# Optimization experiments

Hardware: AMD Instinct MI355X
Metric: run time of the kernel (lower is better)

## Reference

```python
import jax, jax.numpy as jnp
import numpy as np

EPS = 1e-12  # matches torch F.normalize default eps

def l2norm(t):
    n = jnp.linalg.norm(t, axis=-1, keepdims=True)
    return t / jnp.maximum(n, EPS)

def rotate_half(x):
    # '... (j d) -> ... j d' with j=2: split into two halves, return cat(-x2, x1)
    x1, x2 = jnp.split(x, 2, axis=-1)
    return jnp.concatenate((-x2, x1), axis=-1)

def rotary_freqs(seq_len, dim):
    inv_freq = 1.0 / (10000.0 ** (jnp.arange(0, dim, 2, dtype=jnp.float32) / dim))
    seq = jnp.arange(seq_len, dtype=jnp.float32)
    freqs = seq[:, None] * inv_freq[None, :]          # [n, d/2]
    emb = jnp.concatenate((freqs, freqs), axis=-1)    # [n, d]
    return emb[None, None]                            # [1, 1, n, d]

def apply_rotary_pos_emb(t, freqs):
    # rot_dim == dim_head here, so the pass-through slice is empty
    return t * jnp.cos(freqs) + rotate_half(t) * jnp.sin(freqs)

def setup_inputs() -> dict:
    key = jax.random.key(0)
    kq, kk, kv = jax.random.split(key, 3)
    b, h, n, d = 2, 16, 2048, 64
    q = jax.random.normal(kq, (b, h, n, d), dtype=jnp.float32)
    k = jax.random.normal(kk, (b, h, n, d), dtype=jnp.float32)
    v = jax.random.normal(kv, (b, h, n, d), dtype=jnp.float32)
    q_scale = jnp.ones((d,), dtype=jnp.float32)
    k_scale = jnp.ones((d,), dtype=jnp.float32)
    return {"q": q, "k": k, "v": v, "q_scale": q_scale, "k_scale": k_scale}

def reference(q, k, v, q_scale, k_scale):
    b, h, n, d = q.shape
    # QK RMSNorm (l2 normalize + learned per-dim scale)
    q = l2norm(q) * q_scale
    k = l2norm(k) * k_scale
    # rotary position embedding (always applied in the source module)
    freqs = rotary_freqs(n, d)
    q = apply_rotary_pos_emb(q, freqs)
    k = apply_rotary_pos_emb(k, freqs)
    # attention: explicit scores -> softmax -> values
    scale = d ** -0.5
    sim = jnp.einsum('bhid,bhjd->bhij', q, k) * scale
    attn = jax.nn.softmax(sim, axis=-1)
    out = jnp.einsum('bhij,bhjd->bhid', attn, v)
    # 'b h n d -> b n (h d)'
    return out.transpose(0, 2, 1, 3).reshape(b, n, h * d)
```

## Files before the change

kernel.cpp:

```cpp
#include <hip/hip_runtime.h>
#include <math.h>

#define BH   32
#define NSEQ 2048
#define DH   64
#define NH   16
#define LOG2E 1.44269504088896f

typedef _Float16 f16x8 __attribute__((ext_vector_type(8)));
typedef __fp16   fp16x2 __attribute__((ext_vector_type(2)));
typedef float    f32x16v __attribute__((ext_vector_type(16)));
typedef unsigned uint2v __attribute__((ext_vector_type(2)));

#if __has_builtin(__builtin_amdgcn_exp2f)
#define EXP2F(x) __builtin_amdgcn_exp2f(x)
#else
#define EXP2F(x) exp2f(x)
#endif

static __device__ __forceinline__ unsigned pkrtz(float a, float b) {
    fp16x2 r = __builtin_amdgcn_cvt_pkrtz(a, b);
    return __builtin_bit_cast(unsigned, r);
}
static __device__ __forceinline__ unsigned packh_rne(float a, float b) {
    union { _Float16 h[2]; unsigned u; } x;
    x.h[0] = (_Float16)a; x.h[1] = (_Float16)b;
    return x.u;
}
#if __has_builtin(__builtin_amdgcn_perm)
#define PERM(a, b, s) __builtin_amdgcn_perm((a), (b), (s))
#else
static __device__ __forceinline__ unsigned PERM(unsigned a, unsigned b, unsigned s) {
    if (s == 0x05040100u) return (b & 0xffffu) | (a << 16);
    return (b >> 16) | (a & 0xffff0000u);
}
#endif

static __device__ __forceinline__ float2 rope_cs(int pos, int p) {
    float invf_rev = EXP2F(-(float)p * (13.287712379549449f / 32.0f)) * 0.15915494309189535f;
    float rev = (float)pos * invf_rev;
    float fr = rev - floorf(rev);
    float th = fr * 6.283185307179586f;
    return make_float2(__cosf(th), __sinf(th));
}

__global__ __launch_bounds__(256) void prep_all(
    const float* __restrict__ q, const float* __restrict__ k, const float* __restrict__ v,
    const float* __restrict__ qs, const float* __restrict__ ksc,
    unsigned* __restrict__ qh, unsigned* __restrict__ kh, unsigned* __restrict__ vt2) {
    const int bid = blockIdx.x;
    const int t = threadIdx.x;
    if (bid < 16384) {
        const bool isq = bid < 8192;
        const float* in = isq ? q : k;
        const float* sc = isq ? qs : ksc;
        unsigned* outp  = isq ? qh : kh;
        const float smul = isq ? 0.125f * LOG2E : 1.0f;
        const int sb = bid & 8191;
        const int w = t >> 6, lane = t & 63;
        const int c = lane & 31, hfr = lane >> 5;
        const int row = sb * 8 + w * 2 + hfr;
        float2 x2 = *(const float2*)(in + (size_t)row * DH + 2 * c);
        float ss = x2.x * x2.x + x2.y * x2.y;
        #pragma unroll
        for (int off = 16; off > 0; off >>= 1) ss += __shfl_xor(ss, off);
        float inv = 1.0f / fmaxf(sqrtf(ss), 1e-12f);
        float2 s2 = *(const float2*)(sc + 2 * c);
        float t0 = x2.x * inv * s2.x;
        float t1 = x2.y * inv * s2.y;
        float p0 = __shfl_xor(t0, 16);
        float p1 = __shfl_xor(t1, 16);
        float r0 = (c < 16) ? -p0 : p0;
        float r1 = (c < 16) ? -p1 : p1;
        int pos = row & (NSEQ - 1);
        int pp = (2 * c) & 31;
        float2 cs0 = rope_cs(pos, pp);
        float2 cs1 = rope_cs(pos, pp + 1);
        float o0 = (t0 * cs0.x + r0 * cs0.y) * smul;
        float o1 = (t1 * cs1.x + r1 * cs1.y) * smul;
        outp[row * 32 + c] = packh_rne(o0, o1);
    } else {
        const int sb = bid - 16384;
        const int kt = sb & 31, bh = sb >> 5;
        __shared__ float Lv[64 * 68];
        #pragma unroll
        for (int i = 0; i < 4; ++i) {
            int chunk = t + 256 * i;
            int r = chunk >> 4, fg = chunk & 15;
            *(float4*)&Lv[r * 68 + fg * 4] =
                *(const float4*)(v + ((size_t)bh * NSEQ + kt * 64 + r) * DH + fg * 4);
        }
        __syncthreads();
        const int dp = t >> 3, kg = t & 7;
        unsigned u[8];
        #pragma unroll
        for (int j = 0; j < 8; ++j) {
            int key = kg * 8 + j;
            float2 f2 = *(const float2*)&Lv[key * 68 + 2 * dp];
            u[j] = pkrtz(f2.x, f2.y);
        }
        unsigned* dst = vt2 + ((size_t)bh * 32 + dp) * NSEQ + kt * 64 + kg * 8;
        *(uint4*)(dst + 0) = make_uint4(u[0], u[1], u[2], u[3]);
        *(uint4*)(dst + 4) = make_uint4(u[4], u[5], u[6], u[7]);
    }
}

__global__ __launch_bounds__(256, 4) void attn_kernel(
    const unsigned* __restrict__ qh, const unsigned* __restrict__ khg,
    const unsigned* __restrict__ vt2, float* __restrict__ out) {

    __shared__ _Float16 Ks[2][64 * 72];
    __shared__ _Float16 Vs[2][64 * 72];

    const int bh = blockIdx.y, qb = blockIdx.x;
    const int tid = threadIdx.x;
    const int w = tid >> 6, lane = tid & 63;
    const int c = lane & 31, hf = lane >> 5;
    const int qhw = w & 1;
    const int khw = w >> 1;

    const _Float16* qbase = (const _Float16*)qh + ((size_t)bh * NSEQ + qb * 64) * DH;
    const _Float16* kbase = (const _Float16*)khg + (size_t)bh * NSEQ * DH;
    const unsigned* vbase = vt2 + (size_t)bh * 32 * NSEQ;

    #pragma unroll
    for (int i = 0; i < 2; ++i) {
        int chunk = tid + 256 * i;
        int r = chunk >> 3, sg = chunk & 7;
        *(uint4*)&Ks[0][r * 72 + sg * 8] = *(const uint4*)(kbase + r * DH + sg * 8);
    }
    #pragma unroll
    for (int i = 0; i < 2; ++i) {
        int chunk = tid + 256 * i;
        int dp = chunk >> 4, kq = (chunk & 15) * 4;
        uint4 vr = *(const uint4*)(vbase + (size_t)dp * NSEQ + kq);
        uint2 lo, hi;
        lo.x = PERM(vr.y, vr.x, 0x05040100u); hi.x = PERM(vr.y, vr.x, 0x07060302u);
        lo.y = PERM(vr.w, vr.z, 0x05040100u); hi.y = PERM(vr.w, vr.z, 0x07060302u);
        *(uint2*)&Vs[0][(2 * dp) * 72 + kq]     = lo;
        *(uint2*)&Vs[0][(2 * dp + 1) * 72 + kq] = hi;
    }

    f16x8 qf[4];
    #pragma unroll
    for (int ks = 0; ks < 4; ++ks)
        qf[ks] = *(const f16x8*)(qbase + (qhw * 32 + c) * DH + ks * 16 + hf * 8);

    f32x16v o[2];
    #pragma unroll
    for (int mt = 0; mt < 2; ++mt)
        #pragma unroll
        for (int r = 0; r < 16; ++r) o[mt][r] = 0.f;
    float lpart = 0.f;

    __syncthreads();

    for (int jt = 0; jt < 32; ++jt) {
        const int cur = jt & 1;
        uint4 kpre[2], vpre[2];
        if (jt + 1 < 32) {
            #pragma unroll
            for (int i = 0; i < 2; ++i) {
                int chunk = tid + 256 * i;
                int r = chunk >> 3, sg = chunk & 7;
                kpre[i] = *(const uint4*)(kbase + (size_t)(jt + 1) * 64 * DH + r * DH + sg * 8);
            }
            #pragma unroll
            for (int i = 0; i < 2; ++i) {
                int chunk = tid + 256 * i;
                int dp = chunk >> 4, kq = (chunk & 15) * 4;
                vpre[i] = *(const uint4*)(vbase + (size_t)dp * NSEQ + (jt + 1) * 64 + kq);
            }
        }

        f32x16v s;
        #pragma unroll
        for (int r = 0; r < 16; ++r) s[r] = 0.f;
        #pragma unroll
        for (int ks = 0; ks < 4; ++ks) {
            f16x8 ka = *(const f16x8*)&Ks[cur][(khw * 32 + c) * 72 + ks * 16 + hf * 8];
            s = __builtin_amdgcn_mfma_f32_32x32x16_f16(ka, qf[ks], s, 0, 0, 0);
        }

        #pragma unroll
        for (int r = 0; r < 16; ++r) {
            float pv = EXP2F(s[r]);
            s[r] = pv;
            lpart += pv;
        }

        #pragma unroll
        for (int kk = 0; kk < 2; ++kk) {
            unsigned P01 = pkrtz(s[kk * 8 + 0], s[kk * 8 + 1]);
            unsigned P23 = pkrtz(s[kk * 8 + 2], s[kk * 8 + 3]);
            unsigned P45 = pkrtz(s[kk * 8 + 4], s[kk * 8 + 5]);
            unsigned P67 = pkrtz(s[kk * 8 + 6], s[kk * 8 + 7]);
            union { unsigned u[4]; f16x8 v; } B;
#if __has_builtin(__builtin_amdgcn_permlane32_swap)
            uint2v r02 = __builtin_amdgcn_permlane32_swap(P01, P45, 0, 0);
            uint2v r13 = __builtin_amdgcn_permlane32_swap(P23, P67, 0, 0);
            B.u[0] = r02[0]; B.u[1] = r13[0]; B.u[2] = r02[1]; B.u[3] = r13[1];
#else
            unsigned x01 = (unsigned)__shfl_xor((int)P01, 32);
            unsigned x23 = (unsigned)__shfl_xor((int)P23, 32);
            unsigned x45 = (unsigned)__shfl_xor((int)P45, 32);
            unsigned x67 = (unsigned)__shfl_xor((int)P67, 32);
            B.u[0] = hf ? x45 : P01;
            B.u[1] = hf ? x67 : P23;
            B.u[2] = hf ? P45 : x01;
            B.u[3] = hf ? P67 : x23;
#endif
            const int kc = khw * 2 + kk;
            f16x8 va0 = *(const f16x8*)&Vs[cur][c * 72 + kc * 16 + hf * 8];
            f16x8 va1 = *(const f16x8*)&Vs[cur][(32 + c) * 72 + kc * 16 + hf * 8];
            o[0] = __builtin_amdgcn_mfma_f32_32x32x16_f16(va0, B.v, o[0], 0, 0, 0);
            o[1] = __builtin_amdgcn_mfma_f32_32x32x16_f16(va1, B.v, o[1], 0, 0, 0);
        }

        if (jt + 1 < 32) {
            #pragma unroll
            for (int i = 0; i < 2; ++i) {
                int chunk = tid + 256 * i;
                int r = chunk >> 3, sg = chunk & 7;
                *(uint4*)&Ks[1 - cur][r * 72 + sg * 8] = kpre[i];
            }
            #pragma unroll
            for (int i = 0; i < 2; ++i) {
                int chunk = tid + 256 * i;
                int dp = chunk >> 4, kq = (chunk & 15) * 4;
                uint2 lo, hi;
                lo.x = PERM(vpre[i].y, vpre[i].x, 0x05040100u); hi.x = PERM(vpre[i].y, vpre[i].x, 0x07060302u);
                lo.y = PERM(vpre[i].w, vpre[i].z, 0x05040100u); hi.y = PERM(vpre[i].w, vpre[i].z, 0x07060302u);
                *(uint2*)&Vs[1 - cur][(2 * dp) * 72 + kq]     = lo;
                *(uint2*)&Vs[1 - cur][(2 * dp + 1) * 72 + kq] = hi;
            }
        }
        __syncthreads();
    }

    float lw = lpart + __shfl_xor(lpart, 32);
    float* Lred = (float*)&Ks[0][0];
    if (w >= 2) {
        const int base = ((w - 2) * 64 + lane) * 33;
        #pragma unroll
        for (int mt = 0; mt < 2; ++mt)
            #pragma unroll
            for (int r = 0; r < 16; ++r) Lred[base + mt * 16 + r] = o[mt][r];
        Lred[base + 32] = lw;
    }
    __syncthreads();
    if (w < 2) {
        const int base = (w * 64 + lane) * 33;
        #pragma unroll
        for (int mt = 0; mt < 2; ++mt)
            #pragma unroll
            for (int r = 0; r < 16; ++r) o[mt][r] += Lred[base + mt * 16 + r];
        lw += Lred[base + 32];
        float invl = 1.0f / lw;
        const int b = bh >> 4, h = bh & 15;
        const int pos = qb * 64 + w * 32 + c;
        float* obase = out + ((size_t)b * NSEQ + pos) * (NH * DH) + h * DH;
        #pragma unroll
        for (int mt = 0; mt < 2; ++mt)
            #pragma unroll
            for (int g = 0; g < 4; ++g) {
                float4 r4 = make_float4(o[mt][g * 4 + 0] * invl, o[mt][g * 4 + 1] * invl,
                                        o[mt][g * 4 + 2] * invl, o[mt][g * 4 + 3] * invl);
                *(float4*)(obase + mt * 32 + g * 8 + hf * 4) = r4;
            }
    }
}

extern "C" void kernel_launch(void* const* d_in, const int* in_sizes, int n_in,
                              void* d_out, int out_size, void* d_ws, size_t ws_size,
                              hipStream_t stream) {
    const float* q  = (const float*)d_in[0];
    const float* k  = (const float*)d_in[1];
    const float* v  = (const float*)d_in[2];
    const float* qs = (const float*)d_in[3];
    const float* ks = (const float*)d_in[4];
    float* outp = (float*)d_out;

    unsigned* qh  = (unsigned*)d_ws;
    unsigned* kh  = qh + (size_t)BH * NSEQ * 32;
    unsigned* vt2 = kh + (size_t)BH * NSEQ * 32;

    prep_all<<<17408, 256, 0, stream>>>(q, k, v, qs, ks, qh, kh, vt2);
    attn_kernel<<<dim3(NSEQ / 64, BH), 256, 0, stream>>>(qh, kh, vt2, outp);
}
```

Measured before the change: 149.0 us.

## Pre-swizzle K and V into MFMA fragment order and load directly to registers

The prep kernel now writes K and transposed V in an MFMA-operand-ready layout, so each lane can load its fragments from global memory with contiguous 16-byte loads. That lets the attention kernel drop the LDS staging buffers, the PERM shuffles and the per-tile __syncthreads, and register double-buffering replaces the shared-memory double buffer. The grid is also flattened and remapped so that blocks sharing a head are spread across groups, and the occupancy hint drops from 4 to 3 to leave room for the extra registers. Each wave now fetches its K/V fragments separately and relies on L2/cache reuse instead of LDS sharing, which increases global load traffic.

Result: faster. 144.6 us (-3.0%).

```diff
diff --git a/kernel.cpp b/kernel.cpp
--- a/kernel.cpp
+++ b/kernel.cpp
@@ -27,14 +27,6 @@
     x.h[0] = (_Float16)a; x.h[1] = (_Float16)b;
     return x.u;
 }
-#if __has_builtin(__builtin_amdgcn_perm)
-#define PERM(a, b, s) __builtin_amdgcn_perm((a), (b), (s))
-#else
-static __device__ __forceinline__ unsigned PERM(unsigned a, unsigned b, unsigned s) {
-    if (s == 0x05040100u) return (b & 0xffffu) | (a << 16);
-    return (b >> 16) | (a & 0xffff0000u);
-}
-#endif
 
 static __device__ __forceinline__ float2 rope_cs(int pos, int p) {
     float invf_rev = EXP2F(-(float)p * (13.287712379549449f / 32.0f)) * 0.15915494309189535f;
@@ -54,7 +46,6 @@
         const bool isq = bid < 8192;
         const float* in = isq ? q : k;
         const float* sc = isq ? qs : ksc;
-        unsigned* outp  = isq ? qh : kh;
         const float smul = isq ? 0.125f * LOG2E : 1.0f;
         const int sb = bid & 8191;
         const int w = t >> 6, lane = t & 63;
@@ -78,7 +69,15 @@
         float2 cs1 = rope_cs(pos, pp + 1);
         float o0 = (t0 * cs0.x + r0 * cs0.y) * smul;
         float o1 = (t1 * cs1.x + r1 * cs1.y) * smul;
-        outp[row * 32 + c] = packh_rne(o0, o1);
+        unsigned val = packh_rne(o0, o1);
+        if (isq) {
+            qh[row * 32 + c] = val;
+        } else {
+            const int rloc = row & (NSEQ - 1);
+            const unsigned idx = (unsigned)((rloc >> 5) * 1024 + (c >> 3) * 256
+                               + ((c >> 2) & 1) * 128 + (rloc & 31) * 4 + (c & 3));
+            kh[(size_t)(row >> 11) * 65536 + idx] = val;
+        }
     } else {
         const int sb = bid - 16384;
         const int kt = sb & 31, bh = sb >> 5;
@@ -91,28 +90,87 @@
                 *(const float4*)(v + ((size_t)bh * NSEQ + kt * 64 + r) * DH + fg * 4);
         }
         __syncthreads();
-        const int dp = t >> 3, kg = t & 7;
+        const int d = t & 63, kg = t >> 6;
         unsigned u[8];
         #pragma unroll
         for (int j = 0; j < 8; ++j) {
-            int key = kg * 8 + j;
-            float2 f2 = *(const float2*)&Lv[key * 68 + 2 * dp];
-            u[j] = pkrtz(f2.x, f2.y);
+            int ky = kg * 16 + 2 * j;
+            u[j] = pkrtz(Lv[ky * 68 + d], Lv[(ky + 1) * 68 + d]);
         }
-        unsigned* dst = vt2 + ((size_t)bh * 32 + dp) * NSEQ + kt * 64 + kg * 8;
-        *(uint4*)(dst + 0) = make_uint4(u[0], u[1], u[2], u[3]);
-        *(uint4*)(dst + 4) = make_uint4(u[4], u[5], u[6], u[7]);
-    }
-}
-
-__global__ __launch_bounds__(256, 4) void attn_kernel(
-    const unsigned* __restrict__ qh, const unsigned* __restrict__ khg,
-    const unsigned* __restrict__ vt2, float* __restrict__ out) {
-
-    __shared__ _Float16 Ks[2][64 * 72];
-    __shared__ _Float16 Vs[2][64 * 72];
-
-    const int bh = blockIdx.y, qb = blockIdx.x;
+        const int rh = d >> 5, cc = d & 31;
+        unsigned* dst = vt2 + (size_t)bh * 65536
+                      + (size_t)((kt * 4 + kg) * 2 + rh) * 256 + cc * 4;
+        *(uint4*)(dst)       = make_uint4(u[0], u[1], u[2], u[3]);
+        *(uint4*)(dst + 128) = make_uint4(u[4], u[5], u[6], u[7]);
+    }
+}
+
+static __device__ __forceinline__ f16x8 ld8(const unsigned* p) {
+    return *(const f16x8*)p;
+}
+
+static __device__ __forceinline__ void attn_step(
+    const f16x8 (&kc)[4], const f16x8 (&vc)[4],
+    f16x8 (&kn)[4], f16x8 (&vn)[4],
+    const unsigned* kp, const unsigned* vp, bool pre,
+    const f16x8 (&qf)[4], f32x16v (&o)[2], float& lpart, int hf)
+{
+    if (pre) {
+        #pragma unroll
+        for (int ks = 0; ks < 4; ++ks) kn[ks] = ld8(kp + ks * 256);
+        #pragma unroll
+        for (int kk = 0; kk < 2; ++kk)
+            #pragma unroll
+            for (int rh = 0; rh < 2; ++rh)
+                vn[kk * 2 + rh] = ld8(vp + kk * 512 + rh * 256);
+    }
+    f32x16v s;
+    #pragma unroll
+    for (int r = 0; r < 16; ++r) s[r] = 0.f;
+    #pragma unroll
+    for (int ks = 0; ks < 4; ++ks)
+        s = __builtin_amdgcn_mfma_f32_32x32x16_f16(kc[ks], qf[ks], s, 0, 0, 0);
+    #pragma unroll
+    for (int r = 0; r < 16; ++r) {
+        float pv = EXP2F(s[r]);
+        s[r] = pv;
+        lpart += pv;
+    }
+    #pragma unroll
+    for (int kk = 0; kk < 2; ++kk) {
+        unsigned P01 = pkrtz(s[kk * 8 + 0], s[kk * 8 + 1]);
+        unsigned P23 = pkrtz(s[kk * 8 + 2], s[kk * 8 + 3]);
+        unsigned P45 = pkrtz(s[kk * 8 + 4], s[kk * 8 + 5]);
+        unsigned P67 = pkrtz(s[kk * 8 + 6], s[kk * 8 + 7]);
+        union { unsigned u[4]; f16x8 v; } B;
+#if __has_builtin(__builtin_amdgcn_permlane32_swap)
+        uint2v r02 = __builtin_amdgcn_permlane32_swap(P01, P45, 0, 0);
+        uint2v r13 = __builtin_amdgcn_permlane32_swap(P23, P67, 0, 0);
+        B.u[0] = r02[0]; B.u[1] = r13[0]; B.u[2] = r02[1]; B.u[3] = r13[1];
+#else
+        unsigned x01 = (unsigned)__shfl_xor((int)P01, 32);
+        unsigned x23 = (unsigned)__shfl_xor((int)P23, 32);
+        unsigned x45 = (unsigned)__shfl_xor((int)P45, 32);
+        unsigned x67 = (unsigned)__shfl_xor((int)P67, 32);
+        B.u[0] = hf ? x45 : P01;
+        B.u[1] = hf ? x67 : P23;
+        B.u[2] = hf ? P45 : x01;
+        B.u[3] = hf ? P67 : x23;
+#endif
+        o[0] = __builtin_amdgcn_mfma_f32_32x32x16_f16(vc[kk * 2 + 0], B.v, o[0], 0, 0, 0);
+        o[1] = __builtin_amdgcn_mfma_f32_32x32x16_f16(vc[kk * 2 + 1], B.v, o[1], 0, 0, 0);
+    }
+}
+
+__global__ __launch_bounds__(256, 3) void attn_kernel(
+    const unsigned* __restrict__ qh, const unsigned* __restrict__ kf,
+    const unsigned* __restrict__ vf, float* __restrict__ out) {
+
+    __shared__ float Lred[128 * 33];
+
+    const int flat = (blockIdx.x & 7) * 128 + (blockIdx.x >> 3);
+    const int bh = flat >> 5, qb = flat & 31;
+
     const int tid = threadIdx.x;
     const int w = tid >> 6, lane = tid & 63;
     const int c = lane & 31, hf = lane >> 5;
@@ -120,32 +178,23 @@
     const int khw = w >> 1;
 
     const _Float16* qbase = (const _Float16*)qh + ((size_t)bh * NSEQ + qb * 64) * DH;
-    const _Float16* kbase = (const _Float16*)khg + (size_t)bh * NSEQ * DH;
-    const unsigned* vbase = vt2 + (size_t)bh * 32 * NSEQ;
-
-    #pragma unroll
-    for (int i = 0; i < 2; ++i) {
-        int chunk = tid + 256 * i;
-        int r = chunk >> 3, sg = chunk & 7;
-        *(uint4*)&Ks[0][r * 72 + sg * 8] = *(const uint4*)(kbase + r * DH + sg * 8);
-    }
-    #pragma unroll
-    for (int i = 0; i < 2; ++i) {
-        int chunk = tid + 256 * i;
-        int dp = chunk >> 4, kq = (chunk & 15) * 4;
-        uint4 vr = *(const uint4*)(vbase + (size_t)dp * NSEQ + kq);
-        uint2 lo, hi;
-        lo.x = PERM(vr.y, vr.x, 0x05040100u); hi.x = PERM(vr.y, vr.x, 0x07060302u);
-        lo.y = PERM(vr.w, vr.z, 0x05040100u); hi.y = PERM(vr.w, vr.z, 0x07060302u);
-        *(uint2*)&Vs[0][(2 * dp) * 72 + kq]     = lo;
-        *(uint2*)&Vs[0][(2 * dp + 1) * 72 + kq] = hi;
-    }
-
     f16x8 qf[4];
     #pragma unroll
     for (int ks = 0; ks < 4; ++ks)
         qf[ks] = *(const f16x8*)(qbase + (qhw * 32 + c) * DH + ks * 16 + hf * 8);
 
+    const unsigned* kfb = kf + (size_t)bh * 65536 + khw * 1024 + lane * 4;
+    const unsigned* vfb = vf + (size_t)bh * 65536 + khw * 1024 + lane * 4;
+
+    f16x8 ka[4], va[4], kb[4], vb[4];
+    #pragma unroll
+    for (int ks = 0; ks < 4; ++ks) ka[ks] = ld8(kfb + ks * 256);
+    #pragma unroll
+    for (int kk = 0; kk < 2; ++kk)
+        #pragma unroll
+        for (int rh = 0; rh < 2; ++rh)
+            va[kk * 2 + rh] = ld8(vfb + kk * 512 + rh * 256);
+
     f32x16v o[2];
     #pragma unroll
     for (int mt = 0; mt < 2; ++mt)
@@ -153,93 +202,16 @@
         for (int r = 0; r < 16; ++r) o[mt][r] = 0.f;
     float lpart = 0.f;
 
-    __syncthreads();
-
-    for (int jt = 0; jt < 32; ++jt) {
-        const int cur = jt & 1;
-        uint4 kpre[2], vpre[2];
-        if (jt + 1 < 32) {
-            #pragma unroll
-            for (int i = 0; i < 2; ++i) {
-                int chunk = tid + 256 * i;
-                int r = chunk >> 3, sg = chunk & 7;
-                kpre[i] = *(const uint4*)(kbase + (size_t)(jt + 1) * 64 * DH + r * DH + sg * 8);
-            }
-            #pragma unroll
-            for (int i = 0; i < 2; ++i) {
-                int chunk = tid + 256 * i;
-                int dp = chunk >> 4, kq = (chunk & 15) * 4;
-                vpre[i] = *(const uint4*)(vbase + (size_t)dp * NSEQ + (jt + 1) * 64 + kq);
-            }
-        }
-
-        f32x16v s;
-        #pragma unroll
-        for (int r = 0; r < 16; ++r) s[r] = 0.f;
-        #pragma unroll
-        for (int ks = 0; ks < 4; ++ks) {
-            f16x8 ka = *(const f16x8*)&Ks[cur][(khw * 32 + c) * 72 + ks * 16 + hf * 8];
-            s = __builtin_amdgcn_mfma_f32_32x32x16_f16(ka, qf[ks], s, 0, 0, 0);
-        }
-
-        #pragma unroll
-        for (int r = 0; r < 16; ++r) {
-            float pv = EXP2F(s[r]);
-            s[r] = pv;
-            lpart += pv;
-        }
-
-        #pragma unroll
-        for (int kk = 0; kk < 2; ++kk) {
-            unsigned P01 = pkrtz(s[kk * 8 + 0], s[kk * 8 + 1]);
-            unsigned P23 = pkrtz(s[kk * 8 + 2], s[kk * 8 + 3]);
-            unsigned P45 = pkrtz(s[kk * 8 + 4], s[kk * 8 + 5]);
-            unsigned P67 = pkrtz(s[kk * 8 + 6], s[kk * 8 + 7]);
-            union { unsigned u[4]; f16x8 v; } B;
-#if __has_builtin(__builtin_amdgcn_permlane32_swap)
-            uint2v r02 = __builtin_amdgcn_permlane32_swap(P01, P45, 0, 0);
-            uint2v r13 = __builtin_amdgcn_permlane32_swap(P23, P67, 0, 0);
-            B.u[0] = r02[0]; B.u[1] = r13[0]; B.u[2] = r02[1]; B.u[3] = r13[1];
-#else
-            unsigned x01 = (unsigned)__shfl_xor((int)P01, 32);
-            unsigned x23 = (unsigned)__shfl_xor((int)P23, 32);
-            unsigned x45 = (unsigned)__shfl_xor((int)P45, 32);
-            unsigned x67 = (unsigned)__shfl_xor((int)P67, 32);
-            B.u[0] = hf ? x45 : P01;
-            B.u[1] = hf ? x67 : P23;
-            B.u[2] = hf ? P45 : x01;
-            B.u[3] = hf ? P67 : x23;
-#endif
-            const int kc = khw * 2 + kk;
-            f16x8 va0 = *(const f16x8*)&Vs[cur][c * 72 + kc * 16 + hf * 8];
-            f16x8 va1 = *(const f16x8*)&Vs[cur][(32 + c) * 72 + kc * 16 + hf * 8];
-            o[0] = __builtin_amdgcn_mfma_f32_32x32x16_f16(va0, B.v, o[0], 0, 0, 0);
-            o[1] = __builtin_amdgcn_mfma_f32_32x32x16_f16(va1, B.v, o[1], 0, 0, 0);
-        }
-
-        if (jt + 1 < 32) {
-            #pragma unroll
-            for (int i = 0; i < 2; ++i) {
-                int chunk = tid + 256 * i;
-                int r = chunk >> 3, sg = chunk & 7;
-                *(uint4*)&Ks[1 - cur][r * 72 + sg * 8] = kpre[i];
-            }
-            #pragma unroll
-            for (int i = 0; i < 2; ++i) {
-                int chunk = tid + 256 * i;
-                int dp = chunk >> 4, kq = (chunk & 15) * 4;
-                uint2 lo, hi;
-                lo.x = PERM(vpre[i].y, vpre[i].x, 0x05040100u); hi.x = PERM(vpre[i].y, vpre[i].x, 0x07060302u);
-                lo.y = PERM(vpre[i].w, vpre[i].z, 0x05040100u); hi.y = PERM(vpre[i].w, vpre[i].z, 0x07060302u);
-                *(uint2*)&Vs[1 - cur][(2 * dp) * 72 + kq]     = lo;
-                *(uint2*)&Vs[1 - cur][(2 * dp + 1) * 72 + kq] = hi;
-            }
-        }
-        __syncthreads();
+    for (int jt = 0; jt < 32; jt += 2) {
+        attn_step(ka, va, kb, vb,
+                  kfb + (size_t)(jt + 1) * 2048, vfb + (size_t)(jt + 1) * 2048,
+                  true, qf, o, lpart, hf);
+        attn_step(kb, vb, ka, va,
+                  kfb + (size_t)(jt + 2) * 2048, vfb + (size_t)(jt + 2) * 2048,
+                  jt + 2 < 32, qf, o, lpart, hf);
     }
 
     float lw = lpart + __shfl_xor(lpart, 32);
-    float* Lred = (float*)&Ks[0][0];
     if (w >= 2) {
         const int base = ((w - 2) * 64 + lane) * 33;
         #pragma unroll
@@ -286,5 +258,5 @@
     unsigned* vt2 = kh + (size_t)BH * NSEQ * 32;
 
     prep_all<<<17408, 256, 0, stream>>>(q, k, v, qs, ks, qh, kh, vt2);
-    attn_kernel<<<dim3(NSEQ / 64, BH), 256, 0, stream>>>(qh, kh, vt2, outp);
-}
+    attn_kernel<<<1024, 256, 0, stream>>>(qh, kh, vt2, outp);
+}
```
